# Kernel tuning notes

Hardware: AMD Instinct MI355X
Metric: run time of the kernel (lower is better)

## Reference

```python
import jax, jax.numpy as jnp
import numpy as np

R = 32          # voxel resolution (init kwarg)
EPS = 0.0       # init kwarg eps


def _norm_coords(coords):
    # coords: [B, 3, N]
    nc = coords - coords.mean(axis=2, keepdims=True)
    # L2 norm over xyz (dim=1), max over points (dim=2)
    denom = jnp.linalg.norm(nc, axis=1, keepdims=True).max(axis=2, keepdims=True) * 2.0 + EPS
    nc = nc / denom + 0.5
    return jnp.clip(nc * R, 0.0, R - 1)  # [B, 3, N] in [0, R-1]


def setup_inputs() -> dict:
    key = jax.random.key(0)
    k1, k2 = jax.random.split(key)
    features = jax.random.normal(k1, (8, 64, 65536), dtype=jnp.float32)
    coords = jax.random.normal(k2, (8, 3, 65536), dtype=jnp.float32)
    return {"features": features, "coords": coords}


def reference(features, coords):
    # features: [B, C, N], coords: [B, 3, N]
    nc = _norm_coords(coords)
    vox = jnp.round(nc).astype(jnp.int32)                      # [B, 3, N]
    flat = (vox[:, 0] * R + vox[:, 1]) * R + vox[:, 2]         # [B, N] flat voxel ids

    def per_batch(f, idx):
        # f: [C, N], idx: [N] -> scatter-mean into R^3 voxels
        sums = jax.ops.segment_sum(f.T, idx, num_segments=R ** 3)            # [R^3, C]
        cnt = jax.ops.segment_sum(jnp.ones(idx.shape, jnp.float32), idx,
                                  num_segments=R ** 3)                        # [R^3]
        return (sums / jnp.maximum(cnt, 1.0)[:, None]).T                      # [C, R^3]

    vox_feat = jax.vmap(per_batch)(features, flat)             # [B, C, R^3]
    B, C = features.shape[0], features.shape[1]
    return vox_feat.reshape(B, C, R, R, R), nc
```

## Files before the change

kernel.cpp:

```cpp
#include <hip/hip_runtime.h>
#include <hip/hip_fp16.h>

#define RR 32
#define R3 32768
#define NPTS 65536
#define NCH 64
#define NB 8


__global__ void mean1_kernel(const float* __restrict__ coords, double* __restrict__ part) {
    __shared__ double ls[3][4];
    int b = blockIdx.y, blk = blockIdx.x;
    int t = threadIdx.x;
    const float* cb = coords + (size_t)b * 3 * NPTS;
    int base = blk * 1024 + t;
    double sx = 0.0, sy = 0.0, sz = 0.0;
#pragma unroll
    for (int k = 0; k < 4; k++) {
        int n = base + k * 256;
        sx += cb[n];
        sy += cb[NPTS + n];
        sz += cb[2 * NPTS + n];
    }
    for (int off = 32; off > 0; off >>= 1) {
        sx += __shfl_down(sx, off);
        sy += __shfl_down(sy, off);
        sz += __shfl_down(sz, off);
    }
    int wave = t >> 6;
    if ((t & 63) == 0) { ls[0][wave] = sx; ls[1][wave] = sy; ls[2][wave] = sz; }
    __syncthreads();
    if (t == 0) {
        part[((size_t)b * 64 + blk) * 3 + 0] = ls[0][0] + ls[0][1] + ls[0][2] + ls[0][3];
        part[((size_t)b * 64 + blk) * 3 + 1] = ls[1][0] + ls[1][1] + ls[1][2] + ls[1][3];
        part[((size_t)b * 64 + blk) * 3 + 2] = ls[2][0] + ls[2][1] + ls[2][2] + ls[2][3];
    }
}

__global__ void mean2_kernel(const double* __restrict__ part, float* __restrict__ meanf) {
    int b = blockIdx.x, l = threadIdx.x;
    double sx = part[((size_t)b * 64 + l) * 3 + 0];
    double sy = part[((size_t)b * 64 + l) * 3 + 1];
    double sz = part[((size_t)b * 64 + l) * 3 + 2];
    for (int off = 32; off > 0; off >>= 1) {
        sx += __shfl_down(sx, off);
        sy += __shfl_down(sy, off);
        sz += __shfl_down(sz, off);
    }
    if (l == 0) {
        meanf[b * 4 + 0] = (float)(sx * (1.0 / NPTS));
        meanf[b * 4 + 1] = (float)(sy * (1.0 / NPTS));
        meanf[b * 4 + 2] = (float)(sz * (1.0 / NPTS));
    }
}

__global__ void max1_kernel(const float* __restrict__ coords,
                            const float* __restrict__ meanf,
                            float* __restrict__ partmax) {
    __shared__ float ls[4];
    int b = blockIdx.y, blk = blockIdx.x;
    int t = threadIdx.x;
    float mx = meanf[b * 4 + 0], my = meanf[b * 4 + 1], mz = meanf[b * 4 + 2];
    const float* cb = coords + (size_t)b * 3 * NPTS;
    int base = blk * 1024 + t;
    float m = 0.0f;
#pragma unroll
    for (int k = 0; k < 4; k++) {
        int n = base + k * 256;
        float dx = cb[n] - mx;
        float dy = cb[NPTS + n] - my;
        float dz = cb[2 * NPTS + n] - mz;
        m = fmaxf(m, dx * dx + dy * dy + dz * dz);
    }
    for (int off = 32; off > 0; off >>= 1) m = fmaxf(m, __shfl_down(m, off));
    int wave = t >> 6;
    if ((t & 63) == 0) ls[wave] = m;
    __syncthreads();
    if (t == 0) partmax[b * 64 + blk] = fmaxf(fmaxf(ls[0], ls[1]), fmaxf(ls[2], ls[3]));
}

__global__ void max2_kernel(const float* __restrict__ partmax, float* __restrict__ denom) {
    int b = blockIdx.x, l = threadIdx.x;
    float m = partmax[b * 64 + l];
    for (int off = 32; off > 0; off >>= 1) m = fmaxf(m, __shfl_down(m, off));
    if (l == 0) denom[b] = 2.0f * sqrtf(m);
}


__global__ void nc_vid_kernel(const float* __restrict__ coords,
                              const float* __restrict__ meanf,
                              const float* __restrict__ denomv,
                              float* __restrict__ ncout,
                              int* __restrict__ vid,
                              unsigned* __restrict__ cnt) {
    int b = blockIdx.y;
    int n = blockIdx.x * blockDim.x + threadIdx.x;
    float mx = meanf[b * 4 + 0], my = meanf[b * 4 + 1], mz = meanf[b * 4 + 2];
    float denom = denomv[b];
    const float* cb = coords + (size_t)b * 3 * NPTS;
    float dx = cb[n] - mx;
    float dy = cb[NPTS + n] - my;
    float dz = cb[2 * NPTS + n] - mz;
    float qx = fminf(fmaxf((dx / denom + 0.5f) * 32.0f, 0.0f), 31.0f);
    float qy = fminf(fmaxf((dy / denom + 0.5f) * 32.0f, 0.0f), 31.0f);
    float qz = fminf(fmaxf((dz / denom + 0.5f) * 32.0f, 0.0f), 31.0f);
    float* nb_ = ncout + (size_t)b * 3 * NPTS;
    nb_[n] = qx;
    nb_[NPTS + n] = qy;
    nb_[2 * NPTS + n] = qz;
    int flat = ((int)rintf(qx) * RR + (int)rintf(qy)) * RR + (int)rintf(qz);
    vid[b * NPTS + n] = flat;
    atomicAdd(&cnt[b * R3 + flat], 1u);
}

__global__ __launch_bounds__(1024) void scan_kernel(const unsigned* __restrict__ cnt,
                                                    unsigned* __restrict__ cursor) {
    __shared__ unsigned buf[R3 + R3 / 32];
    __shared__ unsigned ls[1024];
    int b = blockIdx.x;
    int t = threadIdx.x;
    const unsigned* c = cnt + b * R3;
    for (int i = t; i < R3; i += 1024) buf[i + (i >> 5)] = c[i];
    __syncthreads();
    int sb = t * 33;
    unsigned v[32];
    unsigned s = 0;
#pragma unroll
    for (int k = 0; k < 32; k++) {
        unsigned x = buf[sb + k];
        v[k] = s;
        s += x;
    }
    ls[t] = s;
    __syncthreads();
    for (int d = 1; d < 1024; d <<= 1) {
        unsigned x = (t >= d) ? ls[t - d] : 0u;
        __syncthreads();
        ls[t] += x;
        __syncthreads();
    }
    unsigned chunk_excl = (t == 0) ? 0u : ls[t - 1];
#pragma unroll
    for (int k = 0; k < 32; k++) buf[sb + k] = chunk_excl + v[k];
    __syncthreads();
    unsigned* cur = cursor + b * R3;
    for (int i = t; i < R3; i += 1024) cur[i] = buf[i + (i >> 5)];
}

__global__ void permute_kernel(const float* __restrict__ feats,
                               const int* __restrict__ vid,
                               unsigned* __restrict__ cursor,
                               __half* __restrict__ ft,
                               int* __restrict__ vid_sorted) {
    __shared__ float tile[64][65];
    __shared__ int spos[64];
    int b  = blockIdx.y;
    int n0 = blockIdx.x * 64;
    int t  = threadIdx.x;

    if (t < 64) {
        int flat = vid[b * NPTS + n0 + t];
        int pos = (int)atomicAdd(&cursor[b * R3 + flat], 1u);
        spos[t] = pos;
        vid_sorted[b * NPTS + pos] = flat;
    }

    const float* fb = feats + (size_t)b * NCH * NPTS + n0;
    int i  = t & 63;
    int c0 = t >> 6;
#pragma unroll
    for (int iter = 0; iter < 16; iter++) {
        int c = iter * 4 + c0;
        tile[i][c] = fb[(size_t)c * NPTS + i];
    }
    __syncthreads();

    int wave = t >> 6;
    int lane = t & 63;
    __half* fbase = ft + (size_t)b * NPTS * NCH + lane;
#pragma unroll
    for (int k = 0; k < 16; k++) {
        int p = wave * 16 + k;
        fbase[(size_t)spos[p] * NCH] = __float2half(tile[p][lane]);
    }
}

__global__ void segsum_kernel(const __half* __restrict__ ft,
                              const int* __restrict__ vid_sorted,
                              float* __restrict__ ws_vox) {
    __shared__ int svid[257];
    int b    = blockIdx.y;
    int t    = threadIdx.x;
    int wave = t >> 6;
    int lane = t & 63;
    int bp0  = blockIdx.x * 256;

    svid[t] = vid_sorted[b * NPTS + bp0 + t];
    if (t == 0)
        svid[256] = (bp0 + 256 < NPTS) ? vid_sorted[b * NPTS + bp0 + 256] : -1;
    __syncthreads();

    int p0 = wave * 64;
    const __half* fb = ft + ((size_t)b * NPTS + bp0 + p0) * NCH + lane;
    float* wv = ws_vox + (size_t)b * R3 * NCH + lane;

    float v[64];
#pragma unroll
    for (int k = 0; k < 64; k++) v[k] = __half2float(fb[(size_t)k * NCH]);

    float s = 0.0f;
    int vcur = svid[p0];
#pragma unroll
    for (int k = 0; k < 64; k++) {
        s += v[k];
        int vnext = svid[p0 + k + 1];
        if (k == 63 && wave == 3) vnext = svid[256];
        if (vnext != vcur) {
            atomicAdd(wv + (size_t)vcur * NCH, s);
            s = 0.0f;
            vcur = vnext;
        }
    }
    if (s != 0.0f) atomicAdd(wv + (size_t)vcur * NCH, s);
}

__global__ void normalize_t_kernel(const float* __restrict__ ws_vox,
                                   const unsigned* __restrict__ cnt,
                                   float* __restrict__ voxout) {
    __shared__ float tile[64][65];
    __shared__ float cinv[64];
    __shared__ unsigned scnt[64];
    int b  = blockIdx.y;
    int v0 = blockIdx.x * 64;
    int t  = threadIdx.x;
    if (t < 64) {
        unsigned c = cnt[b * R3 + v0 + t];
        scnt[t] = c;
        cinv[t] = 1.0f / fmaxf((float)c, 1.0f);
    }
    __syncthreads();
    const float* src = ws_vox + ((size_t)b * R3 + v0) * NCH;
    int c = t & 63;
    int w = t >> 6;
#pragma unroll
    for (int iter = 0; iter < 16; iter++) {
        int vi = iter * 4 + w;
        tile[c][vi] = scnt[vi] ? src[(size_t)vi * NCH + c] * cinv[vi] : 0.0f;
    }
    __syncthreads();
    float* dst = voxout + (size_t)b * NCH * R3 + v0;
    int vi = t & 63;
#pragma unroll
    for (int iter = 0; iter < 16; iter++) {
        int cc = iter * 4 + w;
        dst[(size_t)cc * R3 + vi] = tile[cc][vi];
    }
}


__global__ void scatter_vm_kernel(const float* __restrict__ feats,
                                  const float* __restrict__ coords,
                                  const float* __restrict__ meanf,
                                  const float* __restrict__ denomv,
                                  float* __restrict__ ws_vox,
                                  float* __restrict__ ncout,
                                  float* __restrict__ cnt) {
    __shared__ float tile[64][65];
    __shared__ int   sflat[64];
    int b  = blockIdx.y;
    int n0 = blockIdx.x * 64;
    int t  = threadIdx.x;
    if (t < 64) {
        int n = n0 + t;
        float mx = meanf[b * 4 + 0], my = meanf[b * 4 + 1], mz = meanf[b * 4 + 2];
        float denom = denomv[b];
        const float* cb = coords + (size_t)b * 3 * NPTS;
        float dx = cb[n] - mx;
        float dy = cb[NPTS + n] - my;
        float dz = cb[2 * NPTS + n] - mz;
        float qx = fminf(fmaxf((dx / denom + 0.5f) * 32.0f, 0.0f), 31.0f);
        float qy = fminf(fmaxf((dy / denom + 0.5f) * 32.0f, 0.0f), 31.0f);
        float qz = fminf(fmaxf((dz / denom + 0.5f) * 32.0f, 0.0f), 31.0f);
        float* nb_ = ncout + (size_t)b * 3 * NPTS;
        nb_[n] = qx;
        nb_[NPTS + n] = qy;
        nb_[2 * NPTS + n] = qz;
        int flat = ((int)rintf(qx) * RR + (int)rintf(qy)) * RR + (int)rintf(qz);
        sflat[t] = flat;
        atomicAdd(&cnt[b * R3 + flat], 1.0f);
    }
    const float* fb = feats + (size_t)b * NCH * NPTS + n0;
    int i = t & 63;
    int c0 = t >> 6;
#pragma unroll
    for (int iter = 0; iter < 16; iter++) {
        int c = iter * 4 + c0;
        tile[i][c] = fb[(size_t)c * NPTS + i];
    }
    __syncthreads();
    int wave = t >> 6;
    int lane = t & 63;
#pragma unroll
    for (int k = 0; k < 16; k++) {
        int p = wave * 16 + k;
        float v = tile[p][lane];
        size_t base = ((size_t)b * R3 + sflat[p]) * NCH;
        atomicAdd(&ws_vox[base + lane], v);
    }
}

__global__ void normalize_tf_kernel(const float* __restrict__ ws_vox,
                                    const float* __restrict__ cnt,
                                    float* __restrict__ voxout) {
    __shared__ float tile[64][65];
    __shared__ float cinv[64];
    int b  = blockIdx.y;
    int v0 = blockIdx.x * 64;
    int t  = threadIdx.x;
    if (t < 64) cinv[t] = 1.0f / fmaxf(cnt[b * R3 + v0 + t], 1.0f);
    __syncthreads();
    const float* src = ws_vox + ((size_t)b * R3 + v0) * NCH;
    int c = t & 63;
    int w = t >> 6;
#pragma unroll
    for (int iter = 0; iter < 16; iter++) {
        int vi = iter * 4 + w;
        tile[c][vi] = src[(size_t)vi * NCH + c] * cinv[vi];
    }
    __syncthreads();
    float* dst = voxout + (size_t)b * NCH * R3 + v0;
    int vi = t & 63;
#pragma unroll
    for (int iter = 0; iter < 16; iter++) {
        int cc = iter * 4 + w;
        dst[(size_t)cc * R3 + vi] = tile[cc][vi];
    }
}

extern "C" void kernel_launch(void* const* d_in, const int* in_sizes, int n_in,
                              void* d_out, int out_size, void* d_ws, size_t ws_size,
                              hipStream_t stream) {
    const float* feats  = (const float*)d_in[0];
    const float* coords = (const float*)d_in[1];
    float* out = (float*)d_out;
    float* voxout = out;
    float* ncout  = out + (size_t)NB * NCH * R3;

    double* part    = (double*)d_ws;
    float*  partmax = (float*)((char*)d_ws + 12544);
    float*  meanf   = (float*)((char*)d_ws + 14592);
    float*  denomv  = (float*)((char*)d_ws + 14720);

    const size_t off_cnt   = 16384;
    const size_t cnt_bytes = (size_t)NB * R3 * 4;
    const size_t off_vox   = off_cnt + cnt_bytes;
    const size_t vox_bytes = (size_t)NB * R3 * NCH * 4;
    const size_t off_cur   = off_vox + vox_bytes;
    const size_t off_vid   = off_cur + cnt_bytes;
    const size_t vid_bytes = (size_t)NB * NPTS * 4;
    const size_t off_vs    = off_vid + vid_bytes;
    const size_t off_ft    = off_vs + vid_bytes;
    const size_t ft_bytes  = (size_t)NB * NPTS * NCH * 2;
    const size_t need_sort = off_ft + ft_bytes;
    const size_t need_vm   = off_vox + vox_bytes;

    if (ws_size >= need_sort) {
        unsigned* cnt    = (unsigned*)((char*)d_ws + off_cnt);
        float*    ws_vox = (float*)((char*)d_ws + off_vox);
        unsigned* cursor = (unsigned*)((char*)d_ws + off_cur);
        int*      vid    = (int*)((char*)d_ws + off_vid);
        int*      vid_s  = (int*)((char*)d_ws + off_vs);
        __half*   ft     = (__half*)((char*)d_ws + off_ft);

        hipMemsetAsync((char*)d_ws + off_cnt, 0, cnt_bytes + vox_bytes, stream);

        mean1_kernel<<<dim3(64, NB), 256, 0, stream>>>(coords, part);
        mean2_kernel<<<NB, 64, 0, stream>>>(part, meanf);
        max1_kernel <<<dim3(64, NB), 256, 0, stream>>>(coords, meanf, partmax);
        max2_kernel <<<NB, 64, 0, stream>>>(partmax, denomv);
        nc_vid_kernel<<<dim3(NPTS / 256, NB), 256, 0, stream>>>(coords, meanf, denomv,
                                                                ncout, vid, cnt);
        scan_kernel  <<<NB, 1024, 0, stream>>>(cnt, cursor);
        permute_kernel<<<dim3(NPTS / 64, NB), 256, 0, stream>>>(feats, vid, cursor, ft, vid_s);
        segsum_kernel <<<dim3(NPTS / 256, NB), 256, 0, stream>>>(ft, vid_s, ws_vox);
        normalize_t_kernel<<<dim3(R3 / 64, NB), 256, 0, stream>>>(ws_vox, cnt, voxout);
    } else if (ws_size >= need_vm) {
        float* cntf   = (float*)((char*)d_ws + off_cnt);
        float* ws_vox = (float*)((char*)d_ws + off_vox);
        hipMemsetAsync((char*)d_ws + off_cnt, 0, cnt_bytes + vox_bytes, stream);
        mean1_kernel<<<dim3(64, NB), 256, 0, stream>>>(coords, part);
        mean2_kernel<<<NB, 64, 0, stream>>>(part, meanf);
        max1_kernel <<<dim3(64, NB), 256, 0, stream>>>(coords, meanf, partmax);
        max2_kernel <<<NB, 64, 0, stream>>>(partmax, denomv);
        scatter_vm_kernel<<<dim3(NPTS / 64, NB), 256, 0, stream>>>(
            feats, coords, meanf, denomv, ws_vox, ncout, cntf);
        normalize_tf_kernel<<<dim3(R3 / 64, NB), 256, 0, stream>>>(ws_vox, cntf, voxout);
    }
}
```

Baseline: 329.9 us.

## Fuse segment sum and normalization into per-voxel-bucket kernel with shared accumulation

Replaces the global-atomic segmented sum plus separate normalize/transpose kernel with one kernel where each block owns 32 consecutive voxels, walks their sorted point range, accumulates into shared memory, and writes the normalized output directly. This removes the 64 MB float voxel workspace, its memset, and the global atomics and round-trip reads. In exchange, work per block depends on how many points fall in its voxel range, so load can be uneven, and the sequential tile loop may limit parallelism for dense buckets.

```diff
diff --git a/kernel.cpp b/kernel.cpp
--- a/kernel.cpp
+++ b/kernel.cpp
@@ -1,5 +1,6 @@
 #include <hip/hip_runtime.h>
 #include <hip/hip_fp16.h>
+#include <climits>
 
 #define RR 32
 #define R3 32768
@@ -185,75 +186,68 @@
     }
 }
 
-__global__ void segsum_kernel(const __half* __restrict__ ft,
+__global__ void bucket_kernel(const __half* __restrict__ ft,
                               const int* __restrict__ vid_sorted,
-                              float* __restrict__ ws_vox) {
-    __shared__ int svid[257];
-    int b    = blockIdx.y;
-    int t    = threadIdx.x;
+                              const unsigned* __restrict__ cursor,
+                              const unsigned* __restrict__ cnt,
+                              float* __restrict__ voxout) {
+    __shared__ float acc[32 * NCH];
+    __shared__ float cinv[32];
+    __shared__ int sv[256];
+    int b  = blockIdx.y;
+    int g  = blockIdx.x;
+    int v0 = g * 32;
+    int t  = threadIdx.x;
     int wave = t >> 6;
     int lane = t & 63;
-    int bp0  = blockIdx.x * 256;
-
-    svid[t] = vid_sorted[b * NPTS + bp0 + t];
-    if (t == 0)
-        svid[256] = (bp0 + 256 < NPTS) ? vid_sorted[b * NPTS + bp0 + 256] : -1;
-    __syncthreads();
-
-    int p0 = wave * 64;
-    const __half* fb = ft + ((size_t)b * NPTS + bp0 + p0) * NCH + lane;
-    float* wv = ws_vox + (size_t)b * R3 * NCH + lane;
-
-    float v[64];
-#pragma unroll
-    for (int k = 0; k < 64; k++) v[k] = __half2float(fb[(size_t)k * NCH]);
-
-    float s = 0.0f;
-    int vcur = svid[p0];
-#pragma unroll
-    for (int k = 0; k < 64; k++) {
-        s += v[k];
-        int vnext = svid[p0 + k + 1];
-        if (k == 63 && wave == 3) vnext = svid[256];
-        if (vnext != vcur) {
-            atomicAdd(wv + (size_t)vcur * NCH, s);
-            s = 0.0f;
-            vcur = vnext;
+
+#pragma unroll
+    for (int k = 0; k < 8; k++) acc[t + k * 256] = 0.0f;
+    if (t < 32) cinv[t] = 1.0f / fmaxf((float)cnt[b * R3 + v0 + t], 1.0f);
+
+    unsigned start = (v0 == 0) ? 0u : cursor[b * R3 + v0 - 1];
+    unsigned end   = cursor[b * R3 + v0 + 31];
+    __syncthreads();
+
+    const int* vs = vid_sorted + (size_t)b * NPTS;
+
+    for (unsigned tile0 = start; tile0 < end; tile0 += 256) {
+        unsigned p = tile0 + t;
+        sv[t] = (p < end) ? vs[p] : INT_MAX;
+        __syncthreads();
+
+        int p0 = wave * 64;
+        unsigned pg = tile0 + p0;
+        const __half* fb = ft + ((size_t)b * NPTS + pg) * NCH + lane;
+
+        float v[64];
+#pragma unroll
+        for (int k = 0; k < 64; k++)
+            v[k] = (pg + k < end) ? __half2float(fb[(size_t)k * NCH]) : 0.0f;
+
+        float s = 0.0f;
+        int vcur = sv[p0];
+#pragma unroll
+        for (int k = 0; k < 64; k++) {
+            s += v[k];
+            int vnext = (k == 63) ? -2 : sv[p0 + k + 1];
+            if (vnext != vcur) {
+                if (vcur != INT_MAX)
+                    atomicAdd(&acc[(vcur & 31) * NCH + lane], s);
+                s = 0.0f;
+                vcur = vnext;
+            }
         }
-    }
-    if (s != 0.0f) atomicAdd(wv + (size_t)vcur * NCH, s);
-}
-
-__global__ void normalize_t_kernel(const float* __restrict__ ws_vox,
-                                   const unsigned* __restrict__ cnt,
-                                   float* __restrict__ voxout) {
-    __shared__ float tile[64][65];
-    __shared__ float cinv[64];
-    __shared__ unsigned scnt[64];
-    int b  = blockIdx.y;
-    int v0 = blockIdx.x * 64;
-    int t  = threadIdx.x;
-    if (t < 64) {
-        unsigned c = cnt[b * R3 + v0 + t];
-        scnt[t] = c;
-        cinv[t] = 1.0f / fmaxf((float)c, 1.0f);
-    }
-    __syncthreads();
-    const float* src = ws_vox + ((size_t)b * R3 + v0) * NCH;
-    int c = t & 63;
-    int w = t >> 6;
-#pragma unroll
-    for (int iter = 0; iter < 16; iter++) {
-        int vi = iter * 4 + w;
-        tile[c][vi] = scnt[vi] ? src[(size_t)vi * NCH + c] * cinv[vi] : 0.0f;
-    }
-    __syncthreads();
+        __syncthreads();
+    }
+
     float* dst = voxout + (size_t)b * NCH * R3 + v0;
-    int vi = t & 63;
-#pragma unroll
-    for (int iter = 0; iter < 16; iter++) {
-        int cc = iter * 4 + w;
-        dst[(size_t)cc * R3 + vi] = tile[cc][vi];
+    int qz = t & 31;
+    int c0 = t >> 5;
+#pragma unroll
+    for (int it = 0; it < 8; it++) {
+        int c = it * 8 + c0;
+        dst[(size_t)c * R3 + qz] = acc[qz * NCH + c] * cinv[qz];
     }
 }
 
@@ -353,26 +347,26 @@
 
     const size_t off_cnt   = 16384;
     const size_t cnt_bytes = (size_t)NB * R3 * 4;
-    const size_t off_vox   = off_cnt + cnt_bytes;
-    const size_t vox_bytes = (size_t)NB * R3 * NCH * 4;
-    const size_t off_cur   = off_vox + vox_bytes;
+    const size_t off_cur   = off_cnt + cnt_bytes;
     const size_t off_vid   = off_cur + cnt_bytes;
     const size_t vid_bytes = (size_t)NB * NPTS * 4;
     const size_t off_vs    = off_vid + vid_bytes;
     const size_t off_ft    = off_vs + vid_bytes;
     const size_t ft_bytes  = (size_t)NB * NPTS * NCH * 2;
     const size_t need_sort = off_ft + ft_bytes;
+
+    const size_t off_vox   = off_cnt + cnt_bytes;
+    const size_t vox_bytes = (size_t)NB * R3 * NCH * 4;
     const size_t need_vm   = off_vox + vox_bytes;
 
     if (ws_size >= need_sort) {
         unsigned* cnt    = (unsigned*)((char*)d_ws + off_cnt);
-        float*    ws_vox = (float*)((char*)d_ws + off_vox);
         unsigned* cursor = (unsigned*)((char*)d_ws + off_cur);
         int*      vid    = (int*)((char*)d_ws + off_vid);
         int*      vid_s  = (int*)((char*)d_ws + off_vs);
         __half*   ft     = (__half*)((char*)d_ws + off_ft);
 
-        hipMemsetAsync((char*)d_ws + off_cnt, 0, cnt_bytes + vox_bytes, stream);
+        hipMemsetAsync((char*)d_ws + off_cnt, 0, cnt_bytes, stream);
 
         mean1_kernel<<<dim3(64, NB), 256, 0, stream>>>(coords, part);
         mean2_kernel<<<NB, 64, 0, stream>>>(part, meanf);
@@ -382,8 +376,7 @@
                                                                 ncout, vid, cnt);
         scan_kernel  <<<NB, 1024, 0, stream>>>(cnt, cursor);
         permute_kernel<<<dim3(NPTS / 64, NB), 256, 0, stream>>>(feats, vid, cursor, ft, vid_s);
-        segsum_kernel <<<dim3(NPTS / 256, NB), 256, 0, stream>>>(ft, vid_s, ws_vox);
-        normalize_t_kernel<<<dim3(R3 / 64, NB), 256, 0, stream>>>(ws_vox, cnt, voxout);
+        bucket_kernel <<<dim3(RR * RR, NB), 256, 0, stream>>>(ft, vid_s, cursor, cnt, voxout);
     } else if (ws_size >= need_vm) {
         float* cntf   = (float*)((char*)d_ws + off_cnt);
         float* ws_vox = (float*)((char*)d_ws + off_vox);
```

Result: slower. 513.8 us (+55.7%).
